# Kernel optimization log

Hardware: AMD Instinct MI355X
Metric: run time of the kernel (lower is better)

The kernel has to match this reference:

```python
import jax, jax.numpy as jnp
import numpy as np

EPSILON = 1e-06
REG_STRENGTH = 1.0
KL_FACTOR = 1.0
N_CLASSES = 4
Z_DIM = 32
G_EMBED = 2
N_GROUPS = 16
N_FREQS = 64
N_ROIS = 32
BATCH = 1024


def setup_inputs() -> dict:
    key = jax.random.key(0)
    ks = jax.random.split(key, 16)
    n_feat = N_FREQS * N_ROIS * N_ROIS
    features = jax.random.normal(ks[0], (BATCH, N_FREQS, N_ROIS, N_ROIS), dtype=jnp.float32)
    labels = jax.random.randint(ks[1], (BATCH,), 0, N_CLASSES)
    groups = jax.random.randint(ks[2], (BATCH,), 0, N_GROUPS)
    weights = jax.random.uniform(ks[3], (BATCH,), dtype=jnp.float32)
    noise = jax.random.normal(ks[4], (BATCH, Z_DIM), dtype=jnp.float32)
    # learned parameters (torch Linear weights stored as [in, out])
    s1 = 1.0 / np.sqrt(n_feat + G_EMBED)
    group_embed = jax.random.normal(ks[5], (N_GROUPS, G_EMBED), dtype=jnp.float32)
    W1 = jax.random.uniform(ks[6], (n_feat + G_EMBED, Z_DIM), minval=-s1, maxval=s1, dtype=jnp.float32)
    b1 = jax.random.uniform(ks[7], (Z_DIM,), minval=-s1, maxval=s1, dtype=jnp.float32)
    W2 = jax.random.uniform(ks[8], (n_feat + G_EMBED, Z_DIM), minval=-s1, maxval=s1, dtype=jnp.float32)
    b2 = jax.random.uniform(ks[9], (Z_DIM,), minval=-s1, maxval=s1, dtype=jnp.float32)
    freq_factors = jax.random.normal(ks[10], (N_GROUPS, Z_DIM, N_FREQS), dtype=jnp.float32)
    roi_1_factors = jax.random.normal(ks[11], (N_GROUPS, Z_DIM, N_ROIS), dtype=jnp.float32)
    roi_2_factors = jax.random.normal(ks[12], (N_GROUPS, Z_DIM, N_ROIS), dtype=jnp.float32)
    s2 = 1.0 / np.sqrt(Z_DIM)
    lin_W = jax.random.uniform(ks[13], (Z_DIM, Z_DIM), minval=-s2, maxval=s2, dtype=jnp.float32)
    lin_b = jax.random.uniform(ks[14], (Z_DIM,), minval=-s2, maxval=s2, dtype=jnp.float32)
    logit_bias = jnp.zeros((1, N_CLASSES), dtype=jnp.float32)
    return {
        "features": features, "labels": labels, "groups": groups, "weights": weights,
        "noise": noise, "group_embed": group_embed, "W1": W1, "b1": b1, "W2": W2, "b2": b2,
        "freq_factors": freq_factors, "roi_1_factors": roi_1_factors,
        "roi_2_factors": roi_2_factors, "lin_W": lin_W, "lin_b": lin_b,
        "logit_bias": logit_bias,
    }


def reference(features, labels, groups, weights, noise, group_embed, W1, b1, W2, b2,
              freq_factors, roi_1_factors, roi_2_factors, lin_W, lin_b, logit_bias):
    b = features.shape[0]
    flat = features.reshape(b, -1)                               # [b, f*r*r]
    aug = jnp.concatenate([flat, group_embed[groups]], axis=1)   # [b, nfeat+e]
    z_mu = aug @ W1 + b1                                         # [b, z]
    z_log_std = aug @ W2 + b2
    sigma = EPSILON + jnp.exp(z_log_std)
    # KL(N(mu, sigma) || N(0, 1)), summed over z
    kld = jnp.sum(-jnp.log(sigma) + 0.5 * (sigma * sigma + z_mu * z_mu - 1.0), axis=1)
    zs = z_mu + sigma * noise                                    # rsample
    zs = zs @ lin_W + lin_b
    # CP reconstruction with softplus-positive factors
    freq_f = jax.nn.softplus(freq_factors)                       # [g, z, f]
    roi_1_f = jax.nn.softplus(roi_1_factors)                     # [g, z, r]
    roi_2_f = jax.nn.softplus(roi_2_factors)
    freq_loss = jnp.var(freq_f, axis=0, ddof=1).mean(axis=1).sum()
    roi_loss = (jnp.var(roi_1_f, axis=0, ddof=1) + jnp.var(roi_2_f, axis=0, ddof=1)).mean(axis=1).sum()
    volume = jnp.einsum('bz,bzf,bzr,bzs->bfrs', jax.nn.softplus(zs),
                        freq_f[groups], roi_1_f[groups], roi_2_f[groups])
    rec_loss = REG_STRENGTH * jnp.mean((flat - volume.reshape(b, -1)) ** 2, axis=1)
    logits = jnp.concatenate([zs[:, :N_CLASSES - 1], jnp.ones((b, 1), zs.dtype)], axis=1) + logit_bias
    log_probs = jax.nn.log_softmax(logits, axis=1)[jnp.arange(b), labels]
    loss = jnp.mean(rec_loss - weights * log_probs + KL_FACTOR * kld) + freq_loss + roi_loss
    return loss
```

## Files before the change

kernel.cpp:

```cpp
#include <hip/hip_runtime.h>
#include <math.h>

#define NFEAT 65536
#define KS1   32
#define NTILE 32

#define WS_Z     0
#define WS_T     65536
#define WS_SS    98304
#define WS_SCAL  99328
#define WS_FSP   99392
#define WS_R1SP  132160
#define WS_R2SP  148544
#define WS_G     164928
#define WS_LOSSB 181312
#define WS_SORTI 182336

typedef __bf16 bf16x8 __attribute__((ext_vector_type(8)));
typedef float  floatx4 __attribute__((ext_vector_type(4)));

__device__ __forceinline__ float softplusf(float x) {
    return fmaxf(x, 0.f) + log1pf(expf(-fabsf(x)));
}

__global__ __launch_bounds__(256) void k_sort(const int* __restrict__ groups,
                                              float* __restrict__ wsf) {
    int* order = (int*)(wsf + WS_SORTI);
    int* tg = order + 2048; int* tb = order + 2080; int* tc = order + 2112;
    __shared__ int cnt[16], pos[16];
    int t = threadIdx.x;
    if (t < 16) cnt[t] = 0;
    __syncthreads();
    for (int i = t; i < 1024; i += 256) atomicAdd(&cnt[groups[i]], 1);
    __syncthreads();
    if (t == 0) {
        int tt = 0, base = 0;
        for (int g = 0; g < 16; g++) {
            pos[g] = base;
            int c = cnt[g];
            int nt = (c + 63) >> 6;
            for (int j = 0; j < nt; j++) {
                tg[tt] = g; tb[tt] = base + j * 64;
                int rem = c - j * 64;
                tc[tt] = rem < 64 ? rem : 64;
                tt++;
            }
            base += c;
        }
        for (; tt < NTILE; tt++) { tg[tt] = 0; tb[tt] = 0; tc[tt] = 0; }
    }
    __syncthreads();
    for (int i = t; i < 1024; i += 256) {
        int s = atomicAdd(&pos[groups[i]], 1);
        order[s] = i;
    }
    for (int i = 1024 + t; i < 2048; i += 256) order[i] = 0;
}

__global__ __launch_bounds__(256) void k0_factors(const float* __restrict__ ff,
                                                  const float* __restrict__ r1,
                                                  const float* __restrict__ r2,
                                                  float* __restrict__ ws) {
    int i = blockIdx.x * 256 + threadIdx.x;
    float x;
    if (i < 32768)      x = ff[i];
    else if (i < 49152) x = r1[i - 32768];
    else                x = r2[i - 49152];
    ws[WS_FSP + i] = softplusf(x);
}

__global__ __launch_bounds__(256) void k0_varloss(float* __restrict__ ws) {
    int gid = blockIdx.x * 256 + threadIdx.x;
    float contrib = 0.f;
    if (gid < 2048) {
        const float* F = ws + WS_FSP + gid;
        float sx = 0.f, sx2 = 0.f;
        #pragma unroll
        for (int g = 0; g < 16; g++) { float x = F[g * 2048]; sx += x; sx2 += x * x; }
        contrib = (sx2 - sx * sx * (1.f / 16.f)) * (1.f / 15.f) * (1.f / 64.f);
    } else {
        int p = gid - 2048;
        const float* A = ws + WS_R1SP + p;
        const float* B = ws + WS_R2SP + p;
        float sx = 0.f, sx2 = 0.f, tx = 0.f, tx2 = 0.f;
        #pragma unroll
        for (int g = 0; g < 16; g++) {
            float x = A[g * 1024]; sx += x; sx2 += x * x;
            float y = B[g * 1024]; tx += y; tx2 += y * y;
        }
        contrib = ((sx2 - sx * sx * (1.f / 16.f)) + (tx2 - tx * tx * (1.f / 16.f)))
                  * (1.f / 15.f) * (1.f / 32.f);
    }
    __shared__ float red[256];
    red[threadIdx.x] = contrib;
    __syncthreads();
    for (int o = 128; o > 0; o >>= 1) {
        if (threadIdx.x < o) red[threadIdx.x] += red[threadIdx.x + o];
        __syncthreads();
    }
    if (threadIdx.x == 0)
        atomicAdd(ws + WS_SCAL + (blockIdx.x < 8 ? 0 : 1), red[0]);
}

__global__ __launch_bounds__(256) void k0_gram(float* __restrict__ ws) {
    int g = blockIdx.x, t = threadIdx.x;
    __shared__ float Fg[2048], R1g[1024], R2g[1024];
    for (int i = t; i < 2048; i += 256) Fg[i] = ws[WS_FSP + g * 2048 + i];
    for (int i = t; i < 1024; i += 256) {
        R1g[i] = ws[WS_R1SP + g * 1024 + i];
        R2g[i] = ws[WS_R2SP + g * 1024 + i];
    }
    __syncthreads();
    for (int p = t; p < 1024; p += 256) {
        int z1 = p >> 5, z2 = p & 31;
        float dF = 0.f;
        for (int f = 0; f < 64; f++) dF += Fg[z1 * 64 + f] * Fg[z2 * 64 + f];
        float d1 = 0.f, d2 = 0.f;
        for (int r = 0; r < 32; r++) {
            d1 += R1g[z1 * 32 + r] * R1g[z2 * 32 + r];
            d2 += R2g[z1 * 32 + r] * R2g[z2 * 32 + r];
        }
        ws[WS_G + g * 1024 + p] = dF * d1 * d2;
    }
}

__global__ __launch_bounds__(256) void k_fused(const float* __restrict__ feat,
                                               const float* __restrict__ W1,
                                               const float* __restrict__ W2,
                                               float* __restrict__ wsf) {
    const int rt = blockIdx.x, ks = blockIdx.y;
    const int* order = (const int*)(wsf + WS_SORTI);
    const int tcnt = order[2112 + rt];
    if (tcnt == 0) return;
    const int g     = order[2048 + rt];
    const int tbase = order[2080 + rt];

    __shared__ __bf16 Bsm[2][12800];
    const int tid = threadIdx.x;
    const int w = tid >> 6, lane = tid & 63;
    const int fn = lane & 15, q4 = lane >> 4;
    const size_t kbase = (size_t)ks * 2048;

    const int rowit = w * 16 + fn;
    const int bA = order[tbase + rowit];
    const float* fp = feat + (size_t)bA * NFEAT + kbase + q4 * 8;

    const int sn = tid & 31, sarr = (tid >> 5) & 1, skg8 = tid >> 6;
    const float* Wp = (sarr ? W2 : W1) + kbase * 32 + sn;

    const int kz = tid & 31, kg8 = tid >> 5;
    const int h = kg8 >> 1;
    float r2v[16];
    {
        const float* R2g = wsf + WS_R2SP + g * 1024 + kz * 32 + (kg8 & 1) * 16;
        float4 a0 = *(const float4*)(R2g);
        float4 a1 = *(const float4*)(R2g + 4);
        float4 a2 = *(const float4*)(R2g + 8);
        float4 a3 = *(const float4*)(R2g + 12);
        r2v[0]=a0.x; r2v[1]=a0.y; r2v[2]=a0.z; r2v[3]=a0.w;
        r2v[4]=a1.x; r2v[5]=a1.y; r2v[6]=a1.z; r2v[7]=a1.w;
        r2v[8]=a2.x; r2v[9]=a2.y; r2v[10]=a2.z; r2v[11]=a2.w;
        r2v[12]=a3.x; r2v[13]=a3.y; r2v[14]=a3.z; r2v[15]=a3.w;
    }
    const float* Fzp  = wsf + WS_FSP  + g * 2048 + kz * 64 + ks * 2;
    const float* R1zp = wsf + WS_R1SP + g * 1024 + kz * 32;

    float4 rA[2][8];
    float  rB[4][8];

    #pragma unroll
    for (int kq = 0; kq < 4; kq++) {
        rA[0][kq * 2]     = *(const float4*)(fp + kq * 32);
        rA[0][kq * 2 + 1] = *(const float4*)(fp + kq * 32 + 4);
    }
    #pragma unroll
    for (int p = 0; p < 4; p++) {
        int kg = p * 4 + skg8;
        #pragma unroll
        for (int j = 0; j < 8; j++) rB[p][j] = Wp[(size_t)(kg * 8 + j) * 32];
    }
    {
        float Fv = Fzp[0], R1v = R1zp[h];
        #pragma unroll
        for (int p = 0; p < 4; p++) {
            int kg = p * 4 + skg8;
            bf16x8 pk;
            #pragma unroll
            for (int j = 0; j < 8; j++) pk[j] = (__bf16)rB[p][j];
            *(bf16x8*)&Bsm[0][(kg * 100 + sarr * 32 + sn) * 8] = pk;
        }
        float cf = Fv * R1v;
        #pragma unroll
        for (int ih = 0; ih < 2; ih++) {
            bf16x8 pk;
            #pragma unroll
            for (int j = 0; j < 8; j++) pk[j] = (__bf16)(cf * r2v[ih * 8 + j]);
            *(bf16x8*)&Bsm[0][((kg8 * 2 + ih) * 100 + 64 + kz) * 8] = pk;
        }
    }
    __syncthreads();

    floatx4 acc0 = {0,0,0,0}, acc1 = {0,0,0,0}, acc2 = {0,0,0,0};
    floatx4 acc3 = {0,0,0,0}, acc4 = {0,0,0,0}, acc5 = {0,0,0,0};
    float ssl = 0.f;

    #pragma unroll 2
    for (int cc = 0; cc < 16; cc++) {
        const int cur = cc & 1, nxt = cur ^ 1;
        float FvN = 0.f, R1vN = 0.f;
        if (cc < 15) {
            const float* fpn = fp + (cc + 1) * 128;
            #pragma unroll
            for (int kq = 0; kq < 4; kq++) {
                rA[nxt][kq * 2]     = *(const float4*)(fpn + kq * 32);
                rA[nxt][kq * 2 + 1] = *(const float4*)(fpn + kq * 32 + 4);
            }
            const float* wpn = Wp + (size_t)(cc + 1) * 128 * 32;
            #pragma unroll
            for (int p = 0; p < 4; p++) {
                int kg = p * 4 + skg8;
                #pragma unroll
                for (int j = 0; j < 8; j++) rB[p][j] = wpn[(size_t)(kg * 8 + j) * 32];
            }
            FvN  = Fzp[(cc + 1) >> 3];
            R1vN = R1zp[((cc + 1) & 7) * 4 + h];
        }
        #pragma unroll
        for (int kq = 0; kq < 4; kq++) {
            float4 lo = rA[cur][kq * 2], hi = rA[cur][kq * 2 + 1];
            ssl += lo.x*lo.x + lo.y*lo.y + lo.z*lo.z + lo.w*lo.w
                 + hi.x*hi.x + hi.y*hi.y + hi.z*hi.z + hi.w*hi.w;
            bf16x8 af;
            af[0]=(__bf16)lo.x; af[1]=(__bf16)lo.y; af[2]=(__bf16)lo.z; af[3]=(__bf16)lo.w;
            af[4]=(__bf16)hi.x; af[5]=(__bf16)hi.y; af[6]=(__bf16)hi.z; af[7]=(__bf16)hi.w;
            const __bf16* bb = &Bsm[cur][((kq * 4 + q4) * 100 + fn) * 8];
            bf16x8 b0 = *(const bf16x8*)(bb);
            bf16x8 b1 = *(const bf16x8*)(bb + 16 * 8);
            bf16x8 b2 = *(const bf16x8*)(bb + 32 * 8);
            bf16x8 b3 = *(const bf16x8*)(bb + 48 * 8);
            bf16x8 b4 = *(const bf16x8*)(bb + 64 * 8);
            bf16x8 b5 = *(const bf16x8*)(bb + 80 * 8);
            acc0 = __builtin_amdgcn_mfma_f32_16x16x32_bf16(af, b0, acc0, 0, 0, 0);
            acc1 = __builtin_amdgcn_mfma_f32_16x16x32_bf16(af, b1, acc1, 0, 0, 0);
            acc2 = __builtin_amdgcn_mfma_f32_16x16x32_bf16(af, b2, acc2, 0, 0, 0);
            acc3 = __builtin_amdgcn_mfma_f32_16x16x32_bf16(af, b3, acc3, 0, 0, 0);
            acc4 = __builtin_amdgcn_mfma_f32_16x16x32_bf16(af, b4, acc4, 0, 0, 0);
            acc5 = __builtin_amdgcn_mfma_f32_16x16x32_bf16(af, b5, acc5, 0, 0, 0);
        }
        if (cc < 15) {
            #pragma unroll
            for (int p = 0; p < 4; p++) {
                int kg = p * 4 + skg8;
                bf16x8 pk;
                #pragma unroll
                for (int j = 0; j < 8; j++) pk[j] = (__bf16)rB[p][j];
                *(bf16x8*)&Bsm[nxt][(kg * 100 + sarr * 32 + sn) * 8] = pk;
            }
            float cf = FvN * R1vN;
            #pragma unroll
            for (int ih = 0; ih < 2; ih++) {
                bf16x8 pk;
                #pragma unroll
                for (int j = 0; j < 8; j++) pk[j] = (__bf16)(cf * r2v[ih * 8 + j]);
                *(bf16x8*)&Bsm[nxt][((kg8 * 2 + ih) * 100 + 64 + kz) * 8] = pk;
            }
            __syncthreads();
        }
    }

    float ssv = ssl + __shfl_xor(ssl, 16, 64);
    ssv += __shfl_xor(ssv, 32, 64);
    if (q4 == 0 && rowit < tcnt) atomicAdd(wsf + WS_SS + bA, ssv);

    #pragma unroll
    for (int r = 0; r < 4; r++) {
        int rit = w * 16 + q4 * 4 + r;
        if (rit < tcnt) {
            int b = order[tbase + rit];
            atomicAdd(wsf + WS_Z + b * 64 +  0 + fn, acc0[r]);
            atomicAdd(wsf + WS_Z + b * 64 + 16 + fn, acc1[r]);
            atomicAdd(wsf + WS_Z + b * 64 + 32 + fn, acc2[r]);
            atomicAdd(wsf + WS_Z + b * 64 + 48 + fn, acc3[r]);
            atomicAdd(wsf + WS_T + b * 32 +  0 + fn, acc4[r]);
            atomicAdd(wsf + WS_T + b * 32 + 16 + fn, acc5[r]);
        }
    }
}

__global__ __launch_bounds__(64) void k3_batch(const float* __restrict__ W1,
                                               const float* __restrict__ W2,
                                               const float* __restrict__ b1,
                                               const float* __restrict__ b2,
                                               const float* __restrict__ gemb,
                                               const float* __restrict__ noise,
                                               const float* __restrict__ linW,
                                               const float* __restrict__ linb,
                                               const float* __restrict__ lbias,
                                               const int* __restrict__ groups,
                                               const int* __restrict__ labels,
                                               const float* __restrict__ weights,
                                               float* __restrict__ ws) {
    const int b = blockIdx.x;
    const int t = threadIdx.x;
    const int g = groups[b];
    float sum = ws[WS_Z + b * 64 + t];

    __shared__ float s_mu[32], s_sig[32], s_zs0[32], s_zs[32], s_P[32], s_red[96];
    float ge0 = gemb[g * 2], ge1 = gemb[g * 2 + 1];
    if (t < 32) {
        s_mu[t] = sum + ge0 * W1[(size_t)65536 * 32 + t] + ge1 * W1[(size_t)65537 * 32 + t] + b1[t];
    } else {
        int c = t - 32;
        float ls = sum + ge0 * W2[(size_t)65536 * 32 + c] + ge1 * W2[(size_t)65537 * 32 + c] + b2[c];
        s_sig[c] = 1e-6f + expf(ls);
    }
    __syncthreads();
    if (t < 32) s_zs0[t] = s_mu[t] + s_sig[t] * noise[b * 32 + t];
    __syncthreads();
    if (t < 32) {
        float d = linb[t];
        for (int i = 0; i < 32; i++) d = fmaf(s_zs0[i], linW[i * 32 + t], d);
        s_zs[t] = d;
        s_P[t] = softplusf(d);
    }
    __syncthreads();
    if (t < 32) {
        float mu = s_mu[t], sg = s_sig[t];
        float kld = -logf(sg) + 0.5f * (sg * sg + mu * mu - 1.f);
        float pt = s_P[t] * ws[WS_T + b * 32 + t];
        const float* Grow = ws + WS_G + g * 1024 + t * 32;
        float gd = 0.f;
        for (int j = 0; j < 32; j++) gd = fmaf(Grow[j], s_P[j], gd);
        s_red[t] = kld; s_red[32 + t] = pt; s_red[64 + t] = s_P[t] * gd;
    }
    __syncthreads();
    if (t == 0) {
        float kld = 0.f, pt = 0.f, pgp = 0.f;
        for (int i = 0; i < 32; i++) { kld += s_red[i]; pt += s_red[32 + i]; pgp += s_red[64 + i]; }
        float rec = (ws[WS_SS + b] - 2.f * pt + pgp) * (1.f / 65536.f);
        float l0 = s_zs[0] + lbias[0], l1 = s_zs[1] + lbias[1];
        float l2 = s_zs[2] + lbias[2], l3 = 1.f + lbias[3];
        float m = fmaxf(fmaxf(l0, l1), fmaxf(l2, l3));
        float lse = m + logf(expf(l0 - m) + expf(l1 - m) + expf(l2 - m) + expf(l3 - m));
        int lb = labels[b];
        float ll = ((lb == 0) ? l0 : (lb == 1) ? l1 : (lb == 2) ? l2 : l3) - lse;
        ws[WS_LOSSB + b] = rec - weights[b] * ll + kld;
    }
}

__global__ __launch_bounds__(256) void k4_final(const float* __restrict__ ws, float* __restrict__ out) {
    __shared__ float red[256];
    int t = threadIdx.x;
    float s = 0.f;
    for (int i = t; i < 1024; i += 256) s += ws[WS_LOSSB + i];
    red[t] = s;
    __syncthreads();
    for (int o = 128; o > 0; o >>= 1) {
        if (t < o) red[t] += red[t + o];
        __syncthreads();
    }
    if (t == 0) out[0] = red[0] * (1.f / 1024.f) + ws[WS_SCAL] + ws[WS_SCAL + 1];
}

extern "C" void kernel_launch(void* const* d_in, const int* in_sizes, int n_in,
                              void* d_out, int out_size, void* d_ws, size_t ws_size,
                              hipStream_t stream) {
    const float* feat    = (const float*)d_in[0];
    const int*   labels  = (const int*)d_in[1];
    const int*   groups  = (const int*)d_in[2];
    const float* weights = (const float*)d_in[3];
    const float* noise   = (const float*)d_in[4];
    const float* gemb    = (const float*)d_in[5];
    const float* W1      = (const float*)d_in[6];
    const float* b1      = (const float*)d_in[7];
    const float* W2      = (const float*)d_in[8];
    const float* b2      = (const float*)d_in[9];
    const float* ff      = (const float*)d_in[10];
    const float* r1f     = (const float*)d_in[11];
    const float* r2f     = (const float*)d_in[12];
    const float* linW    = (const float*)d_in[13];
    const float* linb    = (const float*)d_in[14];
    const float* lbias   = (const float*)d_in[15];
    float* ws = (float*)d_ws;
    float* out = (float*)d_out;

    hipMemsetAsync(ws, 0, 99392 * sizeof(float), stream);

    k_sort<<<1, 256, 0, stream>>>(groups, ws);
    k0_factors<<<256, 256, 0, stream>>>(ff, r1f, r2f, ws);
    k0_varloss<<<12, 256, 0, stream>>>(ws);
    k0_gram<<<16, 256, 0, stream>>>(ws);
    k_fused<<<dim3(NTILE, KS1), 256, 0, stream>>>(feat, W1, W2, ws);
    k3_batch<<<1024, 64, 0, stream>>>(W1, W2, b1, b2, gemb, noise, linW, linb, lbias,
                                      groups, labels, weights, ws);
    k4_final<<<1, 256, 0, stream>>>(ws, out);
}
```

Before: 483.4 us.

## Prepack W1/W2 to bf16, stage via global_load_lds, merge prep kernels

Adds a prep pass that converts W1/W2 once into a bf16 packed layout, plus transposed softplus factor tables. The main GEMM kernel then streams B tiles directly into LDS with global_load_lds, instead of doing strided fp32 loads and converting to bf16 on every block. Feature rows are staged through a swizzled LDS A tile, and the squared-sum is computed per row. The four setup kernels are merged into two launches to cut launch overhead. In exchange, the prep pass must write and then re-read a packed weight copy of about 8 MB each call, and the main loop now runs more, smaller k-steps with more barriers.

```diff
diff --git a/kernel.cpp b/kernel.cpp
--- a/kernel.cpp
+++ b/kernel.cpp
@@ -15,118 +15,146 @@
 #define WS_G     164928
 #define WS_LOSSB 181312
 #define WS_SORTI 182336
+#define WS_FT    184832
+#define WS_R1T   217600
+#define WS_WP    233984
 
 typedef __bf16 bf16x8 __attribute__((ext_vector_type(8)));
+typedef __bf16 bf16x4 __attribute__((ext_vector_type(4)));
 typedef float  floatx4 __attribute__((ext_vector_type(4)));
 
 __device__ __forceinline__ float softplusf(float x) {
     return fmaxf(x, 0.f) + log1pf(expf(-fabsf(x)));
 }
 
-__global__ __launch_bounds__(256) void k_sort(const int* __restrict__ groups,
-                                              float* __restrict__ wsf) {
-    int* order = (int*)(wsf + WS_SORTI);
-    int* tg = order + 2048; int* tb = order + 2080; int* tc = order + 2112;
+__device__ __forceinline__ void glds16(const void* g, void* l) {
+    __builtin_amdgcn_global_load_lds(
+        (const __attribute__((address_space(1))) unsigned int*)g,
+        (__attribute__((address_space(3))) unsigned int*)l, 16, 0, 0);
+}
+
+__global__ __launch_bounds__(256) void k0a(const float* __restrict__ ff,
+                                           const float* __restrict__ r1,
+                                           const float* __restrict__ r2,
+                                           const float* __restrict__ W1,
+                                           const float* __restrict__ W2,
+                                           const int* __restrict__ groups,
+                                           float* __restrict__ ws) {
+    const int bid = blockIdx.x, t = threadIdx.x;
     __shared__ int cnt[16], pos[16];
-    int t = threadIdx.x;
-    if (t < 16) cnt[t] = 0;
-    __syncthreads();
-    for (int i = t; i < 1024; i += 256) atomicAdd(&cnt[groups[i]], 1);
-    __syncthreads();
-    if (t == 0) {
-        int tt = 0, base = 0;
-        for (int g = 0; g < 16; g++) {
-            pos[g] = base;
-            int c = cnt[g];
-            int nt = (c + 63) >> 6;
-            for (int j = 0; j < nt; j++) {
-                tg[tt] = g; tb[tt] = base + j * 64;
-                int rem = c - j * 64;
-                tc[tt] = rem < 64 ? rem : 64;
-                tt++;
+    if (bid < 256) {
+        int i = bid * 256 + t;
+        if (i < 32768) {
+            float sp = softplusf(ff[i]);
+            ws[WS_FSP + i] = sp;
+            int g = i >> 11, z = (i >> 6) & 31, f = i & 63;
+            ws[WS_FT + g * 2048 + f * 32 + z] = sp;
+        } else if (i < 49152) {
+            int ii = i - 32768;
+            float sp = softplusf(r1[ii]);
+            ws[WS_R1SP + ii] = sp;
+            int g = ii >> 10, z = (ii >> 5) & 31, r = ii & 31;
+            ws[WS_R1T + g * 1024 + r * 32 + z] = sp;
+        } else {
+            int ii = i - 49152;
+            ws[WS_R2SP + ii] = softplusf(r2[ii]);
+        }
+    } else if (bid < 2304) {
+        int e = (bid - 256) * 256 + t;
+        int kg = e >> 6, col = e & 63;
+        const float* Wsrc = (col < 32 ? W1 : W2) + (size_t)kg * 256 + (col & 31);
+        bf16x8 o;
+        #pragma unroll
+        for (int j = 0; j < 8; j++) o[j] = (__bf16)Wsrc[j * 32];
+        *(bf16x8*)((__bf16*)(ws + WS_WP) + (size_t)e * 8) = o;
+    } else {
+        int* order = (int*)(ws + WS_SORTI);
+        int* tg = order + 2048; int* tb = order + 2080; int* tc = order + 2112;
+        if (t < 16) cnt[t] = 0;
+        __syncthreads();
+        for (int i = t; i < 1024; i += 256) atomicAdd(&cnt[groups[i]], 1);
+        __syncthreads();
+        if (t == 0) {
+            int tt = 0, base = 0;
+            for (int g = 0; g < 16; g++) {
+                pos[g] = base;
+                int c = cnt[g];
+                int nt = (c + 63) >> 6;
+                for (int j = 0; j < nt; j++) {
+                    tg[tt] = g; tb[tt] = base + j * 64;
+                    int rem = c - j * 64;
+                    tc[tt] = rem < 64 ? rem : 64;
+                    tt++;
+                }
+                base += c;
             }
-            base += c;
-        }
-        for (; tt < NTILE; tt++) { tg[tt] = 0; tb[tt] = 0; tc[tt] = 0; }
-    }
-    __syncthreads();
-    for (int i = t; i < 1024; i += 256) {
-        int s = atomicAdd(&pos[groups[i]], 1);
-        order[s] = i;
-    }
-    for (int i = 1024 + t; i < 2048; i += 256) order[i] = 0;
-}
-
-__global__ __launch_bounds__(256) void k0_factors(const float* __restrict__ ff,
-                                                  const float* __restrict__ r1,
-                                                  const float* __restrict__ r2,
-                                                  float* __restrict__ ws) {
-    int i = blockIdx.x * 256 + threadIdx.x;
-    float x;
-    if (i < 32768)      x = ff[i];
-    else if (i < 49152) x = r1[i - 32768];
-    else                x = r2[i - 49152];
-    ws[WS_FSP + i] = softplusf(x);
-}
-
-__global__ __launch_bounds__(256) void k0_varloss(float* __restrict__ ws) {
-    int gid = blockIdx.x * 256 + threadIdx.x;
-    float contrib = 0.f;
-    if (gid < 2048) {
-        const float* F = ws + WS_FSP + gid;
-        float sx = 0.f, sx2 = 0.f;
-        #pragma unroll
-        for (int g = 0; g < 16; g++) { float x = F[g * 2048]; sx += x; sx2 += x * x; }
-        contrib = (sx2 - sx * sx * (1.f / 16.f)) * (1.f / 15.f) * (1.f / 64.f);
+            for (; tt < NTILE; tt++) { tg[tt] = 0; tb[tt] = 0; tc[tt] = 0; }
+        }
+        __syncthreads();
+        for (int i = t; i < 1024; i += 256) {
+            int s = atomicAdd(&pos[groups[i]], 1);
+            order[s] = i;
+        }
+        for (int i = 1024 + t; i < 2048; i += 256) order[i] = 0;
+    }
+}
+
+__global__ __launch_bounds__(256) void k0b(float* __restrict__ ws) {
+    __shared__ float red[256];
+    __shared__ float Fg[2048], R1g[1024], R2g[1024];
+    const int bid = blockIdx.x, t = threadIdx.x;
+    if (bid < 12) {
+        int gid = bid * 256 + t;
+        float contrib = 0.f;
+        if (gid < 2048) {
+            const float* F = ws + WS_FSP + gid;
+            float sx = 0.f, sx2 = 0.f;
+            #pragma unroll
+            for (int g = 0; g < 16; g++) { float x = F[g * 2048]; sx += x; sx2 += x * x; }
+            contrib = (sx2 - sx * sx * (1.f / 16.f)) * (1.f / 15.f) * (1.f / 64.f);
+        } else {
+            int p = gid - 2048;
+            const float* A = ws + WS_R1SP + p;
+            const float* B = ws + WS_R2SP + p;
+            float sx = 0.f, sx2 = 0.f, tx = 0.f, tx2 = 0.f;
+            #pragma unroll
+            for (int g = 0; g < 16; g++) {
+                float x = A[g * 1024]; sx += x; sx2 += x * x;
+                float y = B[g * 1024]; tx += y; tx2 += y * y;
+            }
+            contrib = ((sx2 - sx * sx * (1.f / 16.f)) + (tx2 - tx * tx * (1.f / 16.f)))
+                      * (1.f / 15.f) * (1.f / 32.f);
+        }
+        red[t] = contrib;
+        __syncthreads();
+        for (int o = 128; o > 0; o >>= 1) {
+            if (t < o) red[t] += red[t + o];
+            __syncthreads();
+        }
+        if (t == 0) atomicAdd(ws + WS_SCAL + (bid < 8 ? 0 : 1), red[0]);
     } else {
-        int p = gid - 2048;
-        const float* A = ws + WS_R1SP + p;
-        const float* B = ws + WS_R2SP + p;
-        float sx = 0.f, sx2 = 0.f, tx = 0.f, tx2 = 0.f;
-        #pragma unroll
-        for (int g = 0; g < 16; g++) {
-            float x = A[g * 1024]; sx += x; sx2 += x * x;
-            float y = B[g * 1024]; tx += y; tx2 += y * y;
-        }
-        contrib = ((sx2 - sx * sx * (1.f / 16.f)) + (tx2 - tx * tx * (1.f / 16.f)))
-                  * (1.f / 15.f) * (1.f / 32.f);
-    }
-    __shared__ float red[256];
-    red[threadIdx.x] = contrib;
-    __syncthreads();
-    for (int o = 128; o > 0; o >>= 1) {
-        if (threadIdx.x < o) red[threadIdx.x] += red[threadIdx.x + o];
-        __syncthreads();
-    }
-    if (threadIdx.x == 0)
-        atomicAdd(ws + WS_SCAL + (blockIdx.x < 8 ? 0 : 1), red[0]);
-}
-
-__global__ __launch_bounds__(256) void k0_gram(float* __restrict__ ws) {
-    int g = blockIdx.x, t = threadIdx.x;
-    __shared__ float Fg[2048], R1g[1024], R2g[1024];
-    for (int i = t; i < 2048; i += 256) Fg[i] = ws[WS_FSP + g * 2048 + i];
-    for (int i = t; i < 1024; i += 256) {
-        R1g[i] = ws[WS_R1SP + g * 1024 + i];
-        R2g[i] = ws[WS_R2SP + g * 1024 + i];
-    }
-    __syncthreads();
-    for (int p = t; p < 1024; p += 256) {
-        int z1 = p >> 5, z2 = p & 31;
-        float dF = 0.f;
-        for (int f = 0; f < 64; f++) dF += Fg[z1 * 64 + f] * Fg[z2 * 64 + f];
-        float d1 = 0.f, d2 = 0.f;
-        for (int r = 0; r < 32; r++) {
-            d1 += R1g[z1 * 32 + r] * R1g[z2 * 32 + r];
-            d2 += R2g[z1 * 32 + r] * R2g[z2 * 32 + r];
-        }
-        ws[WS_G + g * 1024 + p] = dF * d1 * d2;
+        int g = bid - 12;
+        for (int i = t; i < 2048; i += 256) Fg[i] = ws[WS_FSP + g * 2048 + i];
+        for (int i = t; i < 1024; i += 256) {
+            R1g[i] = ws[WS_R1SP + g * 1024 + i];
+            R2g[i] = ws[WS_R2SP + g * 1024 + i];
+        }
+        __syncthreads();
+        for (int p = t; p < 1024; p += 256) {
+            int z1 = p >> 5, z2 = p & 31;
+            float dF = 0.f;
+            for (int f = 0; f < 64; f++) dF += Fg[z1 * 64 + f] * Fg[z2 * 64 + f];
+            float d1 = 0.f, d2 = 0.f;
+            for (int r = 0; r < 32; r++) {
+                d1 += R1g[z1 * 32 + r] * R1g[z2 * 32 + r];
+                d2 += R2g[z1 * 32 + r] * R2g[z2 * 32 + r];
+            }
+            ws[WS_G + g * 1024 + p] = dF * d1 * d2;
+        }
     }
 }
 
 __global__ __launch_bounds__(256) void k_fused(const float* __restrict__ feat,
-                                               const float* __restrict__ W1,
-                                               const float* __restrict__ W2,
                                                float* __restrict__ wsf) {
     const int rt = blockIdx.x, ks = blockIdx.y;
     const int* order = (const int*)(wsf + WS_SORTI);
@@ -135,111 +163,96 @@
     const int g     = order[2048 + rt];
     const int tbase = order[2080 + rt];
 
-    __shared__ __bf16 Bsm[2][12800];
+    __shared__ __bf16 Asm[2][4096];
+    __shared__ __bf16 Bsm[2][6400];
+
     const int tid = threadIdx.x;
-    const int w = tid >> 6, lane = tid & 63;
-    const int fn = lane & 15, q4 = lane >> 4;
-    const size_t kbase = (size_t)ks * 2048;
-
-    const int rowit = w * 16 + fn;
-    const int bA = order[tbase + rowit];
-    const float* fp = feat + (size_t)bA * NFEAT + kbase + q4 * 8;
-
-    const int sn = tid & 31, sarr = (tid >> 5) & 1, skg8 = tid >> 6;
-    const float* Wp = (sarr ? W2 : W1) + kbase * 32 + sn;
-
-    const int kz = tid & 31, kg8 = tid >> 5;
-    const int h = kg8 >> 1;
-    float r2v[16];
+    const int w = tid >> 6, l = tid & 63;
+    const int fn = l & 15, q4 = l >> 4;
+
+    const float* fpA[4];
+    int bAi[4], vA[4];
+    #pragma unroll
+    for (int i = 0; i < 4; i++) {
+        int rit = w * 16 + i * 4 + q4;
+        vA[i] = (rit < tcnt);
+        bAi[i] = order[tbase + rit];
+        fpA[i] = feat + (size_t)bAi[i] * NFEAT + (size_t)ks * 2048 + fn * 4;
+    }
+
+    const int kz = tid & 31, kgT = tid >> 5, hK = kgT >> 2;
+    float r2v[8];
     {
-        const float* R2g = wsf + WS_R2SP + g * 1024 + kz * 32 + (kg8 & 1) * 16;
-        float4 a0 = *(const float4*)(R2g);
-        float4 a1 = *(const float4*)(R2g + 4);
-        float4 a2 = *(const float4*)(R2g + 8);
-        float4 a3 = *(const float4*)(R2g + 12);
+        const float* R2p = wsf + WS_R2SP + g * 1024 + kz * 32 + (kgT & 3) * 8;
+        float4 a0 = *(const float4*)R2p, a1 = *(const float4*)(R2p + 4);
         r2v[0]=a0.x; r2v[1]=a0.y; r2v[2]=a0.z; r2v[3]=a0.w;
         r2v[4]=a1.x; r2v[5]=a1.y; r2v[6]=a1.z; r2v[7]=a1.w;
-        r2v[8]=a2.x; r2v[9]=a2.y; r2v[10]=a2.z; r2v[11]=a2.w;
-        r2v[12]=a3.x; r2v[13]=a3.y; r2v[14]=a3.z; r2v[15]=a3.w;
-    }
-    const float* Fzp  = wsf + WS_FSP  + g * 2048 + kz * 64 + ks * 2;
-    const float* R1zp = wsf + WS_R1SP + g * 1024 + kz * 32;
-
-    float4 rA[2][8];
-    float  rB[4][8];
-
-    #pragma unroll
-    for (int kq = 0; kq < 4; kq++) {
-        rA[0][kq * 2]     = *(const float4*)(fp + kq * 32);
-        rA[0][kq * 2 + 1] = *(const float4*)(fp + kq * 32 + 4);
-    }
-    #pragma unroll
-    for (int p = 0; p < 4; p++) {
-        int kg = p * 4 + skg8;
-        #pragma unroll
-        for (int j = 0; j < 8; j++) rB[p][j] = Wp[(size_t)(kg * 8 + j) * 32];
-    }
-    {
-        float Fv = Fzp[0], R1v = R1zp[h];
-        #pragma unroll
-        for (int p = 0; p < 4; p++) {
-            int kg = p * 4 + skg8;
-            bf16x8 pk;
-            #pragma unroll
-            for (int j = 0; j < 8; j++) pk[j] = (__bf16)rB[p][j];
-            *(bf16x8*)&Bsm[0][(kg * 100 + sarr * 32 + sn) * 8] = pk;
-        }
-        float cf = Fv * R1v;
-        #pragma unroll
-        for (int ih = 0; ih < 2; ih++) {
-            bf16x8 pk;
-            #pragma unroll
-            for (int j = 0; j < 8; j++) pk[j] = (__bf16)(cf * r2v[ih * 8 + j]);
-            *(bf16x8*)&Bsm[0][((kg8 * 2 + ih) * 100 + 64 + kz) * 8] = pk;
-        }
-    }
+    }
+    const float* Ftp  = wsf + WS_FT  + g * 2048 + (ks * 2) * 32 + kz;
+    const float* R1tp = wsf + WS_R1T + g * 1024 + kz;
+
+    const __bf16* wp = (const __bf16*)(wsf + WS_WP);
+    const size_t kgbase = (size_t)ks * 256;
+
+    const float4 f4z = make_float4(0.f, 0.f, 0.f, 0.f);
+    float4 vA4[4];
+    float ssl[4] = {0.f, 0.f, 0.f, 0.f};
+
+#define ISSUE(buf, cc) do { \
+    glds16(wp + ((kgbase + (size_t)(cc) * 8 + (size_t)w) * 64 + (size_t)l) * 8, \
+           &Bsm[buf][w * 800]); \
+    glds16(wp + ((kgbase + (size_t)(cc) * 8 + 4 + (size_t)w) * 64 + (size_t)l) * 8, \
+           &Bsm[buf][(4 + w) * 800]); \
+    vA4[0] = vA[0] ? *(const float4*)(fpA[0] + (cc) * 64) : f4z; \
+    vA4[1] = vA[1] ? *(const float4*)(fpA[1] + (cc) * 64) : f4z; \
+    vA4[2] = vA[2] ? *(const float4*)(fpA[2] + (cc) * 64) : f4z; \
+    vA4[3] = vA[3] ? *(const float4*)(fpA[3] + (cc) * 64) : f4z; \
+} while (0)
+
+#define ASTORE(buf, i) do { \
+    float4 v = vA4[i]; \
+    ssl[i] += v.x * v.x + v.y * v.y + v.z * v.z + v.w * v.w; \
+    const int row_ = w * 16 + (i) * 4 + q4; \
+    const int byt_ = (row_ * 128 + fn * 8) ^ ((row_ & 7) << 4); \
+    bf16x4 a_; a_[0] = (__bf16)v.x; a_[1] = (__bf16)v.y; \
+    a_[2] = (__bf16)v.z; a_[3] = (__bf16)v.w; \
+    *(bf16x4*)((char*)&Asm[buf][0] + byt_) = a_; \
+} while (0)
+
+#define WSTAGE(buf, cc) do { \
+    float cf_ = Ftp[((cc) >> 4) * 32] * R1tp[((((cc) * 2) + hK) & 31) * 32]; \
+    bf16x8 pk_; \
+    pk_[0]=(__bf16)(cf_*r2v[0]); pk_[1]=(__bf16)(cf_*r2v[1]); \
+    pk_[2]=(__bf16)(cf_*r2v[2]); pk_[3]=(__bf16)(cf_*r2v[3]); \
+    pk_[4]=(__bf16)(cf_*r2v[4]); pk_[5]=(__bf16)(cf_*r2v[5]); \
+    pk_[6]=(__bf16)(cf_*r2v[6]); pk_[7]=(__bf16)(cf_*r2v[7]); \
+    *(bf16x8*)&Bsm[buf][(kgT * 100 + 64 + kz) * 8] = pk_; \
+    ASTORE(buf, 0); ASTORE(buf, 1); ASTORE(buf, 2); ASTORE(buf, 3); \
+} while (0)
+
+    ISSUE(0, 0);
+    WSTAGE(0, 0);
     __syncthreads();
 
     floatx4 acc0 = {0,0,0,0}, acc1 = {0,0,0,0}, acc2 = {0,0,0,0};
     floatx4 acc3 = {0,0,0,0}, acc4 = {0,0,0,0}, acc5 = {0,0,0,0};
-    float ssl = 0.f;
-
+
+    const int arow = w * 16 + fn;
     #pragma unroll 2
-    for (int cc = 0; cc < 16; cc++) {
+    for (int cc = 0; cc < 32; cc++) {
         const int cur = cc & 1, nxt = cur ^ 1;
-        float FvN = 0.f, R1vN = 0.f;
-        if (cc < 15) {
-            const float* fpn = fp + (cc + 1) * 128;
-            #pragma unroll
-            for (int kq = 0; kq < 4; kq++) {
-                rA[nxt][kq * 2]     = *(const float4*)(fpn + kq * 32);
-                rA[nxt][kq * 2 + 1] = *(const float4*)(fpn + kq * 32 + 4);
-            }
-            const float* wpn = Wp + (size_t)(cc + 1) * 128 * 32;
-            #pragma unroll
-            for (int p = 0; p < 4; p++) {
-                int kg = p * 4 + skg8;
-                #pragma unroll
-                for (int j = 0; j < 8; j++) rB[p][j] = wpn[(size_t)(kg * 8 + j) * 32];
-            }
-            FvN  = Fzp[(cc + 1) >> 3];
-            R1vN = R1zp[((cc + 1) & 7) * 4 + h];
-        }
+        if (cc < 31) ISSUE(nxt, cc + 1);
         #pragma unroll
-        for (int kq = 0; kq < 4; kq++) {
-            float4 lo = rA[cur][kq * 2], hi = rA[cur][kq * 2 + 1];
-            ssl += lo.x*lo.x + lo.y*lo.y + lo.z*lo.z + lo.w*lo.w
-                 + hi.x*hi.x + hi.y*hi.y + hi.z*hi.z + hi.w*hi.w;
-            bf16x8 af;
-            af[0]=(__bf16)lo.x; af[1]=(__bf16)lo.y; af[2]=(__bf16)lo.z; af[3]=(__bf16)lo.w;
-            af[4]=(__bf16)hi.x; af[5]=(__bf16)hi.y; af[6]=(__bf16)hi.z; af[7]=(__bf16)hi.w;
+        for (int kq = 0; kq < 2; kq++) {
+            int rbyt = (arow * 128 + (kq * 4 + q4) * 16) ^ ((arow & 7) << 4);
+            bf16x8 af = *(const bf16x8*)((const char*)&Asm[cur][0] + rbyt);
             const __bf16* bb = &Bsm[cur][((kq * 4 + q4) * 100 + fn) * 8];
             bf16x8 b0 = *(const bf16x8*)(bb);
-            bf16x8 b1 = *(const bf16x8*)(bb + 16 * 8);
-            bf16x8 b2 = *(const bf16x8*)(bb + 32 * 8);
-            bf16x8 b3 = *(const bf16x8*)(bb + 48 * 8);
-            bf16x8 b4 = *(const bf16x8*)(bb + 64 * 8);
-            bf16x8 b5 = *(const bf16x8*)(bb + 80 * 8);
+            bf16x8 b1 = *(const bf16x8*)(bb + 128);
+            bf16x8 b2 = *(const bf16x8*)(bb + 256);
+            bf16x8 b3 = *(const bf16x8*)(bb + 384);
+            bf16x8 b4 = *(const bf16x8*)(bb + 512);
+            bf16x8 b5 = *(const bf16x8*)(bb + 640);
             acc0 = __builtin_amdgcn_mfma_f32_16x16x32_bf16(af, b0, acc0, 0, 0, 0);
             acc1 = __builtin_amdgcn_mfma_f32_16x16x32_bf16(af, b1, acc1, 0, 0, 0);
             acc2 = __builtin_amdgcn_mfma_f32_16x16x32_bf16(af, b2, acc2, 0, 0, 0);
@@ -247,31 +260,22 @@
             acc4 = __builtin_amdgcn_mfma_f32_16x16x32_bf16(af, b4, acc4, 0, 0, 0);
             acc5 = __builtin_amdgcn_mfma_f32_16x16x32_bf16(af, b5, acc5, 0, 0, 0);
         }
-        if (cc < 15) {
-            #pragma unroll
-            for (int p = 0; p < 4; p++) {
-                int kg = p * 4 + skg8;
-                bf16x8 pk;
-                #pragma unroll
-                for (int j = 0; j < 8; j++) pk[j] = (__bf16)rB[p][j];
-                *(bf16x8*)&Bsm[nxt][(kg * 100 + sarr * 32 + sn) * 8] = pk;
-            }
-            float cf = FvN * R1vN;
-            #pragma unroll
-            for (int ih = 0; ih < 2; ih++) {
-                bf16x8 pk;
-                #pragma unroll
-                for (int j = 0; j < 8; j++) pk[j] = (__bf16)(cf * r2v[ih * 8 + j]);
-                *(bf16x8*)&Bsm[nxt][((kg8 * 2 + ih) * 100 + 64 + kz) * 8] = pk;
-            }
-            __syncthreads();
-        }
-    }
-
-    float ssv = ssl + __shfl_xor(ssl, 16, 64);
-    ssv += __shfl_xor(ssv, 32, 64);
-    if (q4 == 0 && rowit < tcnt) atomicAdd(wsf + WS_SS + bA, ssv);
-
+        if (cc < 31) WSTAGE(nxt, cc + 1);
+        __syncthreads();
+    }
+#undef ISSUE
+#undef ASTORE
+#undef WSTAGE
+
+    #pragma unroll
+    for (int i = 0; i < 4; i++) {
+        float s = ssl[i];
+        s += __shfl_xor(s, 1, 64);
+        s += __shfl_xor(s, 2, 64);
+        s += __shfl_xor(s, 4, 64);
+        s += __shfl_xor(s, 8, 64);
+        if (fn == 0 && vA[i]) atomicAdd(wsf + WS_SS + bAi[i], s);
+    }
     #pragma unroll
     for (int r = 0; r < 4; r++) {
         int rit = w * 16 + q4 * 4 + r;
@@ -386,11 +390,9 @@
 
     hipMemsetAsync(ws, 0, 99392 * sizeof(float), stream);
 
-    k_sort<<<1, 256, 0, stream>>>(groups, ws);
-    k0_factors<<<256, 256, 0, stream>>>(ff, r1f, r2f, ws);
-    k0_varloss<<<12, 256, 0, stream>>>(ws);
-    k0_gram<<<16, 256, 0, stream>>>(ws);
-    k_fused<<<dim3(NTILE, KS1), 256, 0, stream>>>(feat, W1, W2, ws);
+    k0a<<<2305, 256, 0, stream>>>(ff, r1f, r2f, W1, W2, groups, ws);
+    k0b<<<28, 256, 0, stream>>>(ws);
+    k_fused<<<dim3(NTILE, KS1), 256, 0, stream>>>(feat, ws);
     k3_batch<<<1024, 64, 0, stream>>>(W1, W2, b1, b2, gemb, noise, linW, linb, lbias,
                                       groups, labels, weights, ws);
     k4_final<<<1, 256, 0, stream>>>(ws, out);
```

Result: slower. 550.6 us (+13.9%).

## Prepack W1/W2 to bf16 and stream B tiles via global_load_lds

Applied to the files above, without the earlier changes.

A prologue kernel now converts W1/W2 into a bf16 layout matching the shared-memory B tile, and writes transposed copies of the softplus factors. The main fused kernel then loads W directly into LDS with global_load_lds instead of strided fp32 loads, register staging and conversion, and reads the factors coalesced. The small setup kernels (sort, factors, varloss, gram) are merged into two launches. The cost is an extra pass over W every call to write the packed copy, and the barrier now runs on every iteration.

```diff
diff --git a/kernel.cpp b/kernel.cpp
--- a/kernel.cpp
+++ b/kernel.cpp
@@ -15,6 +15,9 @@
 #define WS_G     164928
 #define WS_LOSSB 181312
 #define WS_SORTI 182336
+#define WS_FT    184832
+#define WS_R1T   217600
+#define WS_WP    233984
 
 typedef __bf16 bf16x8 __attribute__((ext_vector_type(8)));
 typedef float  floatx4 __attribute__((ext_vector_type(4)));
@@ -23,110 +26,134 @@
     return fmaxf(x, 0.f) + log1pf(expf(-fabsf(x)));
 }
 
-__global__ __launch_bounds__(256) void k_sort(const int* __restrict__ groups,
-                                              float* __restrict__ wsf) {
-    int* order = (int*)(wsf + WS_SORTI);
-    int* tg = order + 2048; int* tb = order + 2080; int* tc = order + 2112;
+__device__ __forceinline__ void glds16(const void* g, void* l) {
+    __builtin_amdgcn_global_load_lds(
+        (const __attribute__((address_space(1))) unsigned int*)g,
+        (__attribute__((address_space(3))) unsigned int*)l, 16, 0, 0);
+}
+
+__global__ __launch_bounds__(256) void k0a(const float* __restrict__ ff,
+                                           const float* __restrict__ r1,
+                                           const float* __restrict__ r2,
+                                           const float* __restrict__ W1,
+                                           const float* __restrict__ W2,
+                                           const int* __restrict__ groups,
+                                           float* __restrict__ ws) {
+    const int bid = blockIdx.x, t = threadIdx.x;
     __shared__ int cnt[16], pos[16];
-    int t = threadIdx.x;
-    if (t < 16) cnt[t] = 0;
-    __syncthreads();
-    for (int i = t; i < 1024; i += 256) atomicAdd(&cnt[groups[i]], 1);
-    __syncthreads();
-    if (t == 0) {
-        int tt = 0, base = 0;
-        for (int g = 0; g < 16; g++) {
-            pos[g] = base;
-            int c = cnt[g];
-            int nt = (c + 63) >> 6;
-            for (int j = 0; j < nt; j++) {
-                tg[tt] = g; tb[tt] = base + j * 64;
-                int rem = c - j * 64;
-                tc[tt] = rem < 64 ? rem : 64;
-                tt++;
-            }
-            base += c;
-        }
-        for (; tt < NTILE; tt++) { tg[tt] = 0; tb[tt] = 0; tc[tt] = 0; }
-    }
-    __syncthreads();
-    for (int i = t; i < 1024; i += 256) {
-        int s = atomicAdd(&pos[groups[i]], 1);
-        order[s] = i;
-    }
-    for (int i = 1024 + t; i < 2048; i += 256) order[i] = 0;
-}
-
-__global__ __launch_bounds__(256) void k0_factors(const float* __restrict__ ff,
-                                                  const float* __restrict__ r1,
-                                                  const float* __restrict__ r2,
-                                                  float* __restrict__ ws) {
-    int i = blockIdx.x * 256 + threadIdx.x;
-    float x;
-    if (i < 32768)      x = ff[i];
-    else if (i < 49152) x = r1[i - 32768];
-    else                x = r2[i - 49152];
-    ws[WS_FSP + i] = softplusf(x);
-}
-
-__global__ __launch_bounds__(256) void k0_varloss(float* __restrict__ ws) {
-    int gid = blockIdx.x * 256 + threadIdx.x;
-    float contrib = 0.f;
-    if (gid < 2048) {
-        const float* F = ws + WS_FSP + gid;
-        float sx = 0.f, sx2 = 0.f;
+    if (bid < 256) {
+        int i = bid * 256 + t;
+        if (i < 32768) {
+            float sp = softplusf(ff[i]);
+            ws[WS_FSP + i] = sp;
+            int g = i >> 11, z = (i >> 6) & 31, f = i & 63;
+            ws[WS_FT + g * 2048 + f * 32 + z] = sp;
+        } else if (i < 49152) {
+            int ii = i - 32768;
+            float sp = softplusf(r1[ii]);
+            ws[WS_R1SP + ii] = sp;
+            int g = ii >> 10, z = (ii >> 5) & 31, r = ii & 31;
+            ws[WS_R1T + g * 1024 + r * 32 + z] = sp;
+        } else {
+            int ii = i - 49152;
+            ws[WS_R2SP + ii] = softplusf(r2[ii]);
+        }
+    } else if (bid < 2304) {
+        int e = (bid - 256) * 256 + t;
+        int kg = e >> 6, col = e & 63;
+        const float* Wsrc = (col < 32 ? W1 : W2) + (size_t)kg * 256 + (col & 31);
+        bf16x8 o;
         #pragma unroll
-        for (int g = 0; g < 16; g++) { float x = F[g * 2048]; sx += x; sx2 += x * x; }
-        contrib = (sx2 - sx * sx * (1.f / 16.f)) * (1.f / 15.f) * (1.f / 64.f);
+        for (int j = 0; j < 8; j++) o[j] = (__bf16)Wsrc[j * 32];
+        *(bf16x8*)((__bf16*)(ws + WS_WP) + (size_t)e * 8) = o;
     } else {
-        int p = gid - 2048;
-        const float* A = ws + WS_R1SP + p;
-        const float* B = ws + WS_R2SP + p;
-        float sx = 0.f, sx2 = 0.f, tx = 0.f, tx2 = 0.f;
-        #pragma unroll
-        for (int g = 0; g < 16; g++) {
-            float x = A[g * 1024]; sx += x; sx2 += x * x;
-            float y = B[g * 1024]; tx += y; tx2 += y * y;
-        }
-        contrib = ((sx2 - sx * sx * (1.f / 16.f)) + (tx2 - tx * tx * (1.f / 16.f)))
-                  * (1.f / 15.f) * (1.f / 32.f);
-    }
+        int* order = (int*)(ws + WS_SORTI);
+        int* tg = order + 2048; int* tb = order + 2080; int* tc = order + 2112;
+        if (t < 16) cnt[t] = 0;
+        __syncthreads();
+        for (int i = t; i < 1024; i += 256) atomicAdd(&cnt[groups[i]], 1);
+        __syncthreads();
+        if (t == 0) {
+            int tt = 0, base = 0;
+            for (int g = 0; g < 16; g++) {
+                pos[g] = base;
+                int c = cnt[g];
+                int nt = (c + 63) >> 6;
+                for (int j = 0; j < nt; j++) {
+                    tg[tt] = g; tb[tt] = base + j * 64;
+                    int rem = c - j * 64;
+                    tc[tt] = rem < 64 ? rem : 64;
+                    tt++;
+                }
+                base += c;
+            }
+            for (; tt < NTILE; tt++) { tg[tt] = 0; tb[tt] = 0; tc[tt] = 0; }
+        }
+        __syncthreads();
+        for (int i = t; i < 1024; i += 256) {
+            int s = atomicAdd(&pos[groups[i]], 1);
+            order[s] = i;
+        }
+        for (int i = 1024 + t; i < 2048; i += 256) order[i] = 0;
+    }
+}
+
+__global__ __launch_bounds__(256) void k0b(float* __restrict__ ws) {
     __shared__ float red[256];
-    red[threadIdx.x] = contrib;
-    __syncthreads();
-    for (int o = 128; o > 0; o >>= 1) {
-        if (threadIdx.x < o) red[threadIdx.x] += red[threadIdx.x + o];
-        __syncthreads();
-    }
-    if (threadIdx.x == 0)
-        atomicAdd(ws + WS_SCAL + (blockIdx.x < 8 ? 0 : 1), red[0]);
-}
-
-__global__ __launch_bounds__(256) void k0_gram(float* __restrict__ ws) {
-    int g = blockIdx.x, t = threadIdx.x;
     __shared__ float Fg[2048], R1g[1024], R2g[1024];
-    for (int i = t; i < 2048; i += 256) Fg[i] = ws[WS_FSP + g * 2048 + i];
-    for (int i = t; i < 1024; i += 256) {
-        R1g[i] = ws[WS_R1SP + g * 1024 + i];
-        R2g[i] = ws[WS_R2SP + g * 1024 + i];
-    }
-    __syncthreads();
-    for (int p = t; p < 1024; p += 256) {
-        int z1 = p >> 5, z2 = p & 31;
-        float dF = 0.f;
-        for (int f = 0; f < 64; f++) dF += Fg[z1 * 64 + f] * Fg[z2 * 64 + f];
-        float d1 = 0.f, d2 = 0.f;
-        for (int r = 0; r < 32; r++) {
-            d1 += R1g[z1 * 32 + r] * R1g[z2 * 32 + r];
-            d2 += R2g[z1 * 32 + r] * R2g[z2 * 32 + r];
-        }
-        ws[WS_G + g * 1024 + p] = dF * d1 * d2;
+    const int bid = blockIdx.x, t = threadIdx.x;
+    if (bid < 12) {
+        int gid = bid * 256 + t;
+        float contrib = 0.f;
+        if (gid < 2048) {
+            const float* F = ws + WS_FSP + gid;
+            float sx = 0.f, sx2 = 0.f;
+            #pragma unroll
+            for (int g = 0; g < 16; g++) { float x = F[g * 2048]; sx += x; sx2 += x * x; }
+            contrib = (sx2 - sx * sx * (1.f / 16.f)) * (1.f / 15.f) * (1.f / 64.f);
+        } else {
+            int p = gid - 2048;
+            const float* A = ws + WS_R1SP + p;
+            const float* B = ws + WS_R2SP + p;
+            float sx = 0.f, sx2 = 0.f, tx = 0.f, tx2 = 0.f;
+            #pragma unroll
+            for (int g = 0; g < 16; g++) {
+                float x = A[g * 1024]; sx += x; sx2 += x * x;
+                float y = B[g * 1024]; tx += y; tx2 += y * y;
+            }
+            contrib = ((sx2 - sx * sx * (1.f / 16.f)) + (tx2 - tx * tx * (1.f / 16.f)))
+                      * (1.f / 15.f) * (1.f / 32.f);
+        }
+        red[t] = contrib;
+        __syncthreads();
+        for (int o = 128; o > 0; o >>= 1) {
+            if (t < o) red[t] += red[t + o];
+            __syncthreads();
+        }
+        if (t == 0) atomicAdd(ws + WS_SCAL + (bid < 8 ? 0 : 1), red[0]);
+    } else {
+        int g = bid - 12;
+        for (int i = t; i < 2048; i += 256) Fg[i] = ws[WS_FSP + g * 2048 + i];
+        for (int i = t; i < 1024; i += 256) {
+            R1g[i] = ws[WS_R1SP + g * 1024 + i];
+            R2g[i] = ws[WS_R2SP + g * 1024 + i];
+        }
+        __syncthreads();
+        for (int p = t; p < 1024; p += 256) {
+            int z1 = p >> 5, z2 = p & 31;
+            float dF = 0.f;
+            for (int f = 0; f < 64; f++) dF += Fg[z1 * 64 + f] * Fg[z2 * 64 + f];
+            float d1 = 0.f, d2 = 0.f;
+            for (int r = 0; r < 32; r++) {
+                d1 += R1g[z1 * 32 + r] * R1g[z2 * 32 + r];
+                d2 += R2g[z1 * 32 + r] * R2g[z2 * 32 + r];
+            }
+            ws[WS_G + g * 1024 + p] = dF * d1 * d2;
+        }
     }
 }
 
 __global__ __launch_bounds__(256) void k_fused(const float* __restrict__ feat,
-                                               const float* __restrict__ W1,
-                                               const float* __restrict__ W2,
                                                float* __restrict__ wsf) {
     const int rt = blockIdx.x, ks = blockIdx.y;
     const int* order = (const int*)(wsf + WS_SORTI);
@@ -144,9 +171,6 @@
     const int rowit = w * 16 + fn;
     const int bA = order[tbase + rowit];
     const float* fp = feat + (size_t)bA * NFEAT + kbase + q4 * 8;
-
-    const int sn = tid & 31, sarr = (tid >> 5) & 1, skg8 = tid >> 6;
-    const float* Wp = (sarr ? W2 : W1) + kbase * 32 + sn;
 
     const int kz = tid & 31, kg8 = tid >> 5;
     const int h = kg8 >> 1;
@@ -162,11 +186,13 @@
         r2v[8]=a2.x; r2v[9]=a2.y; r2v[10]=a2.z; r2v[11]=a2.w;
         r2v[12]=a3.x; r2v[13]=a3.y; r2v[14]=a3.z; r2v[15]=a3.w;
     }
-    const float* Fzp  = wsf + WS_FSP  + g * 2048 + kz * 64 + ks * 2;
-    const float* R1zp = wsf + WS_R1SP + g * 1024 + kz * 32;
+    const float* Ftp  = wsf + WS_FT  + g * 2048 + (ks * 2) * 32 + kz;
+    const float* R1tp = wsf + WS_R1T + g * 1024 + kz;
+
+    const __bf16* wp = (const __bf16*)(wsf + WS_WP);
+    const size_t kgb = (size_t)ks * 256;
 
     float4 rA[2][8];
-    float  rB[4][8];
 
     #pragma unroll
     for (int kq = 0; kq < 4; kq++) {
@@ -174,22 +200,11 @@
         rA[0][kq * 2 + 1] = *(const float4*)(fp + kq * 32 + 4);
     }
     #pragma unroll
-    for (int p = 0; p < 4; p++) {
-        int kg = p * 4 + skg8;
-        #pragma unroll
-        for (int j = 0; j < 8; j++) rB[p][j] = Wp[(size_t)(kg * 8 + j) * 32];
-    }
+    for (int p = 0; p < 4; p++)
+        glds16(wp + ((kgb + (size_t)(w * 4 + p)) * 64 + (size_t)lane) * 8,
+               &Bsm[0][(w * 4 + p) * 800]);
     {
-        float Fv = Fzp[0], R1v = R1zp[h];
-        #pragma unroll
-        for (int p = 0; p < 4; p++) {
-            int kg = p * 4 + skg8;
-            bf16x8 pk;
-            #pragma unroll
-            for (int j = 0; j < 8; j++) pk[j] = (__bf16)rB[p][j];
-            *(bf16x8*)&Bsm[0][(kg * 100 + sarr * 32 + sn) * 8] = pk;
-        }
-        float cf = Fv * R1v;
+        float cf = Ftp[0] * R1tp[h * 32];
         #pragma unroll
         for (int ih = 0; ih < 2; ih++) {
             bf16x8 pk;
@@ -215,15 +230,12 @@
                 rA[nxt][kq * 2]     = *(const float4*)(fpn + kq * 32);
                 rA[nxt][kq * 2 + 1] = *(const float4*)(fpn + kq * 32 + 4);
             }
-            const float* wpn = Wp + (size_t)(cc + 1) * 128 * 32;
-            #pragma unroll
-            for (int p = 0; p < 4; p++) {
-                int kg = p * 4 + skg8;
-                #pragma unroll
-                for (int j = 0; j < 8; j++) rB[p][j] = wpn[(size_t)(kg * 8 + j) * 32];
-            }
-            FvN  = Fzp[(cc + 1) >> 3];
-            R1vN = R1zp[((cc + 1) & 7) * 4 + h];
+            #pragma unroll
+            for (int p = 0; p < 4; p++)
+                glds16(wp + ((kgb + (size_t)((cc + 1) * 16 + w * 4 + p)) * 64 + (size_t)lane) * 8,
+                       &Bsm[nxt][(w * 4 + p) * 800]);
+            FvN  = Ftp[((cc + 1) >> 3) * 32];
+            R1vN = R1tp[(((cc + 1) & 7) * 4 + h) * 32];
         }
         #pragma unroll
         for (int kq = 0; kq < 4; kq++) {
@@ -248,14 +260,6 @@
             acc5 = __builtin_amdgcn_mfma_f32_16x16x32_bf16(af, b5, acc5, 0, 0, 0);
         }
         if (cc < 15) {
-            #pragma unroll
-            for (int p = 0; p < 4; p++) {
-                int kg = p * 4 + skg8;
-                bf16x8 pk;
-                #pragma unroll
-                for (int j = 0; j < 8; j++) pk[j] = (__bf16)rB[p][j];
-                *(bf16x8*)&Bsm[nxt][(kg * 100 + sarr * 32 + sn) * 8] = pk;
-            }
             float cf = FvN * R1vN;
             #pragma unroll
             for (int ih = 0; ih < 2; ih++) {
@@ -264,8 +268,8 @@
                 for (int j = 0; j < 8; j++) pk[j] = (__bf16)(cf * r2v[ih * 8 + j]);
                 *(bf16x8*)&Bsm[nxt][((kg8 * 2 + ih) * 100 + 64 + kz) * 8] = pk;
             }
-            __syncthreads();
-        }
+        }
+        __syncthreads();
     }
 
     float ssv = ssl + __shfl_xor(ssl, 16, 64);
@@ -386,11 +390,9 @@
 
     hipMemsetAsync(ws, 0, 99392 * sizeof(float), stream);
 
-    k_sort<<<1, 256, 0, stream>>>(groups, ws);
-    k0_factors<<<256, 256, 0, stream>>>(ff, r1f, r2f, ws);
-    k0_varloss<<<12, 256, 0, stream>>>(ws);
-    k0_gram<<<16, 256, 0, stream>>>(ws);
-    k_fused<<<dim3(NTILE, KS1), 256, 0, stream>>>(feat, W1, W2, ws);
+    k0a<<<2305, 256, 0, stream>>>(ff, r1f, r2f, W1, W2, groups, ws);
+    k0b<<<28, 256, 0, stream>>>(ws);
+    k_fused<<<dim3(NTILE, KS1), 256, 0, stream>>>(feat, ws);
     k3_batch<<<1024, 64, 0, stream>>>(W1, W2, b1, b2, gemb, noise, linW, linb, lbias,
                                       groups, labels, weights, ws);
     k4_final<<<1, 256, 0, stream>>>(ws, out);
```

After: 464.5 us. 1.04x faster.
